# Performance work log

Measured on AMD Instinct MI355X. Metric: run time of the kernel, lower is better.

Reference implementation:

```python
import jax, jax.numpy as jnp
import numpy as np

EPS = 1e-8
R_CUT = 4.8
NEW_NB = 20  # hardcoded neighbor truncation in the original forward
B = 32768
NB = 64


def setup_inputs() -> dict:
    key = jax.random.key(0)
    ks = jax.random.split(key, 9)
    # dr: random directions with radii in [1.5, 4.5] so R > ecode (tanh^2 <= 1);
    # this avoids NaN from negative base with fractional exponent (same hazard exists in torch).
    raw = jax.random.normal(ks[0], (B, NB, 3), dtype=jnp.float32)
    direction = raw / jnp.linalg.norm(raw, axis=-1, keepdims=True)
    radius = 1.5 + 3.0 * jax.random.uniform(ks[1], (B, NB, 1), dtype=jnp.float32)
    dr = direction * radius
    orientation = jax.random.normal(ks[2], (B, 3, 3), dtype=jnp.float32)
    n_orientation = jax.random.normal(ks[3], (B, NB, 3, 3), dtype=jnp.float32)

    def lin(k, fan_in, fan_out):
        s = 1.0 / np.sqrt(fan_in)
        kw, kb = jax.random.split(k)
        W = jax.random.uniform(kw, (fan_in, fan_out), jnp.float32, -s, s)
        b = jax.random.uniform(kb, (fan_out,), jnp.float32, -s, s)
        return W, b

    W0, b0 = lin(ks[4], 15, 64)
    W1, b1 = lin(ks[5], 64, 64)
    W2, b2 = lin(ks[6], 64, 1)
    f1 = jax.random.uniform(ks[7], (3, 1), dtype=jnp.float32)
    f2 = jax.random.uniform(ks[8], (3, 1), dtype=jnp.float32)
    return dict(dr=dr, orientation=orientation, n_orientation=n_orientation,
                W0=W0, b0=b0, W1=W1, b1=b1, W2=W2, b2=b2, f1=f1, f2=f2)


def _prior_net(x, W0, b0, W1, b1, W2, b2):
    # Linear-tanh-Linear-tanh-Linear (dropout inactive at eval)
    h = jnp.tanh(x @ W0 + b0)
    h = jnp.tanh(h @ W1 + b1)
    return h @ W2 + b2


def _energy(new_dr_norm, orientation, new_R, new_n_or, fcR, W0, b0, W1, b1, W2, b2, f1, f2):
    b, n = new_dr_norm.shape[:2]
    dr_o = jnp.einsum('bnk,bkh->bnh', new_dr_norm, orientation)            # [B,20,3]
    dr_no = jnp.einsum('bnk,bnkh->bnh', new_dr_norm, new_n_or)             # [B,20,3]
    o_no = jnp.einsum('bhl,bnhm->bnlm', orientation, new_n_or).reshape(b, n, 9)
    feat = jnp.concatenate([dr_o, dr_no, o_no], axis=-1)                   # [B,20,15]
    enc = jnp.tanh(_prior_net(feat, W0, b0, W1, b1, W2, b2))               # [B,20,1]
    ecode = (enc ** 2 + EPS)[..., None, None]                              # [B,20,1,1,1]
    prior = new_R[..., None, None] - ecode                                 # [B,20,1,1,1]
    prior = (f1 ** 2 + EPS) * prior                                        # [B,20,1,3,1]
    prior = prior ** (-(f2 ** 2 + EPS))                                    # power-law
    prior = prior.sum(axis=3).reshape(b, n, 1)                             # [B,20,1]
    energy = prior.sum(axis=1, keepdims=True) * fcR                        # [B,20,1]
    return energy


def _forward(dr, orientation, n_orientation, W0, b0, W1, b1, W2, b2, f1, f2):
    b = dr.shape[0]
    dr = dr + EPS
    R = jnp.linalg.norm(dr, axis=-1, keepdims=True)                        # [B,Nb,1]
    dr_norm = dr / R
    idx = jnp.argsort(R, axis=1)[:, :NEW_NB, :]                            # [B,20,1]
    new_R = jnp.take_along_axis(R, idx, axis=1)                            # [B,20,1]
    new_dr_norm = jnp.take_along_axis(dr_norm, jnp.broadcast_to(idx, (b, NEW_NB, 3)), axis=1)
    new_n_or = jnp.take_along_axis(n_orientation, jnp.broadcast_to(idx[..., None], (b, NEW_NB, 3, 3)), axis=1)
    fcR = jnp.where(new_R > R_CUT, 0.0, 0.5 * jnp.cos(jnp.pi * new_R / R_CUT) + 0.5)

    def esum(ndn, orient):
        e = _energy(ndn, orient, new_R, new_n_or, fcR, W0, b0, W1, b1, W2, b2, f1, f2)
        return e.sum(), e

    # mirrors torch.autograd.grad(energy.sum(), (new_dr_norm, orientation), create_graph=True)
    (_, energy), (g_dr, g_or) = jax.value_and_grad(esum, argnums=(0, 1), has_aux=True)(new_dr_norm, orientation)
    force = g_dr.sum(axis=1)                                               # [B,3]
    torque = (jnp.cross(g_or[:, :, 0], orientation[:, :, 0])
              + jnp.cross(g_or[:, :, 1], orientation[:, :, 1])
              + jnp.cross(g_or[:, :, 2], orientation[:, :, 2]))            # [B,3]
    return force, torque, energy


def reference(dr, orientation, n_orientation, W0, b0, W1, b1, W2, b2, f1, f2):
    return _forward(dr, orientation, n_orientation, W0, b0, W1, b1, W2, b2, f1, f2)
```

## Files before the change

### kernel.cpp

```cpp
#include <hip/hip_runtime.h>

#define EPSF 1e-8f
#define RCUT 4.8f
#define NB 64
#define NSEL 20

#define OW0T 0
#define OB0  1024
#define OB1  1088
#define OW2  1152
#define OB2  1216
#define OAQ  1220
#define OCQ  1224
#define OLG  1228
#define OW1  1232
#define WSWN 5328

__device__ __forceinline__ float fast_tanh(float x) {
    float e = __expf(2.0f * x);
    return 1.0f - __fdividef(2.0f, e + 1.0f);
}

extern "C" __global__ void __launch_bounds__(256)
sel_kernel(const float* __restrict__ dr, const float* __restrict__ n_or,
           const float* __restrict__ W0, const float* __restrict__ b0,
           const float* __restrict__ W1, const float* __restrict__ b1,
           const float* __restrict__ W2, const float* __restrict__ b2,
           const float* __restrict__ f1, const float* __restrict__ f2,
           float* __restrict__ ws_R, float* __restrict__ ws_fc,
           float* __restrict__ ws_F, int* __restrict__ ws_idx,
           float* __restrict__ ws_ndn, float* __restrict__ ws_nor,
           float* __restrict__ wsW)
{
    __shared__ float R_s[256];
    const int t = threadIdx.x;
    const int g = t >> 6;
    const int j = t & 63;
    const int b = blockIdx.x * 4 + g;

    const float* p = dr + ((size_t)b * NB + j) * 3;
    float x = p[0] + EPSF, y = p[1] + EPSF, z = p[2] + EPSF;
    float R = sqrtf(x * x + y * y + z * z);
    R_s[t] = R;
    __syncthreads();

    int rank = 0;
    const float* grp = R_s + g * 64;
    #pragma unroll 8
    for (int k = 0; k < 64; ++k) {
        float Rk = grp[k];
        rank += (Rk < R || (Rk == R && k < j)) ? 1 : 0;
    }

    float fc = 0.0f;
    if (rank < NSEL) {
        fc = (R > RCUT) ? 0.0f
                        : (0.5f * __cosf(3.14159265358979323846f * R / RCUT) + 0.5f);
        size_t o = (size_t)b * NSEL + rank;
        ws_R[o]  = R;
        ws_fc[o] = fc;
        if (ws_idx) ws_idx[o] = j;
        float inv = 1.0f / R;
        ws_ndn[o * 3 + 0] = x * inv;
        ws_ndn[o * 3 + 1] = y * inv;
        ws_ndn[o * 3 + 2] = z * inv;
    }

    if (ws_nor) {
        const float* np = n_or + ((size_t)b * NB + j) * 9;
        float r[9];
        #pragma unroll
        for (int q = 0; q < 9; ++q) r[q] = np[q];
        if (rank < NSEL) {
            float* dst = ws_nor + ((size_t)b * NSEL + rank) * 9;
            #pragma unroll
            for (int q = 0; q < 9; ++q) dst[q] = r[q];
        }
    }

    float F = fc;
    for (int off = 32; off > 0; off >>= 1) F += __shfl_xor(F, off, 64);
    if (j == 0) ws_F[b] = F;

    if (blockIdx.x == 0) {
        for (int i = t; i < 15 * 64; i += 256) {
            int k = i >> 6, jj = i & 63;
            wsW[OW0T + jj * 16 + k] = W0[i];
        }
        for (int i = t; i < 64 * 64; i += 256)
            wsW[OW1 + i] = W1[i];
        if (t < 64) {
            wsW[OB0 + t] = b0[t];
            wsW[OB1 + t] = b1[t];
            wsW[OW2 + t] = W2[t];
        }
        if (t == 0) wsW[OB2] = b2[0];
        if (t < 3) {
            float a = f1[t] * f1[t] + EPSF;
            float c = f2[t] * f2[t] + EPSF;
            wsW[OAQ + t] = a;
            wsW[OCQ + t] = c;
            wsW[OLG + t] = __logf(a);
        }
    }
}

template<bool PRE>
__global__ void __launch_bounds__(320, 4)
energy_kernel_t(const float* __restrict__ orientation,
                const float* __restrict__ n_or,
                const float* __restrict__ wsW,
                const float* __restrict__ wsD,
                const int*   __restrict__ ws_idx_fb,
                const float* __restrict__ ws_ndn_fb,
                float* __restrict__ outBase, const int Bn)
{
    __shared__ float sNr[320 * 9];
    __shared__ float p_s[320];
    __shared__ float red[320][12];
    __shared__ float G[16][12];

    const float* W0T = wsW + OW0T;
    const float* b0  = wsW + OB0;
    const float* b1  = wsW + OB1;
    const float* W2  = wsW + OW2;
    const float* W1  = wsW + OW1;

    const float* ws_R  = wsD;
    const float* ws_fc = wsD + (size_t)Bn * NSEL;
    const float* ws_F  = wsD + (size_t)Bn * (2 * NSEL);
    const float* ws_ndn = PRE ? (wsD + (size_t)Bn * (2 * NSEL + 1)) : ws_ndn_fb;
    const float* ws_nor = wsD + (size_t)Bn * (2 * NSEL + 1 + 3 * NSEL);

    const int t = threadIdx.x;
    const int bl = t / 20;
    const int n  = t % 20;
    const int b  = blockIdx.x * 16 + bl;
    const size_t o = (size_t)b * NSEL + n;

    float feat[15];
    {
        const float nd0 = ws_ndn[o * 3 + 0];
        const float nd1 = ws_ndn[o * 3 + 1];
        const float nd2 = ws_ndn[o * 3 + 2];
        float O[9], Nr[9];
        const float* Op = orientation + (size_t)b * 9;
        #pragma unroll
        for (int i = 0; i < 9; ++i) O[i] = Op[i];
        if (PRE) {
            const float* Np = ws_nor + o * 9;
            #pragma unroll
            for (int i = 0; i < 9; ++i) Nr[i] = Np[i];
        } else {
            const int idx = ws_idx_fb[o];
            const float* Np = n_or + ((size_t)b * NB + idx) * 9;
            #pragma unroll
            for (int i = 0; i < 9; ++i) Nr[i] = Np[i];
        }
        #pragma unroll
        for (int q = 0; q < 9; ++q) sNr[t * 9 + q] = Nr[q];

        #pragma unroll
        for (int h = 0; h < 3; ++h)
            feat[h] = nd0 * O[h] + nd1 * O[3 + h] + nd2 * O[6 + h];
        #pragma unroll
        for (int h = 0; h < 3; ++h)
            feat[3 + h] = nd0 * Nr[h] + nd1 * Nr[3 + h] + nd2 * Nr[6 + h];
        #pragma unroll
        for (int l = 0; l < 3; ++l)
            #pragma unroll
            for (int m = 0; m < 3; ++m)
                feat[6 + l * 3 + m] = O[l] * Nr[m] + O[3 + l] * Nr[3 + m] + O[6 + l] * Nr[6 + m];
    }

    float acc[64];
    #pragma unroll
    for (int i = 0; i < 64; ++i) acc[i] = b1[i];

    for (int j = 0; j < 64; j += 2) {
        const float* w0a = W0T + j * 16;
        const float* w0b = w0a + 16;
        float za = b0[j], zb = b0[j + 1];
        #pragma unroll
        for (int k = 0; k < 15; ++k) {
            za = fmaf(feat[k], w0a[k], za);
            zb = fmaf(feat[k], w0b[k], zb);
        }
        float ha = fast_tanh(za), hb = fast_tanh(zb);
        const float* w1a = W1 + j * 64;
        const float* w1b = w1a + 64;
        #pragma unroll
        for (int i = 0; i < 64; ++i)
            acc[i] = fmaf(hb, w1b[i], fmaf(ha, w1a[i], acc[i]));
    }

    float z30 = wsW[OB2], z31 = 0.f, z32 = 0.f, z33 = 0.f;
    #pragma unroll
    for (int i = 0; i < 64; i += 4) {
        acc[i]     = fast_tanh(acc[i]);
        acc[i + 1] = fast_tanh(acc[i + 1]);
        acc[i + 2] = fast_tanh(acc[i + 2]);
        acc[i + 3] = fast_tanh(acc[i + 3]);
        z30 = fmaf(acc[i],     W2[i],     z30);
        z31 = fmaf(acc[i + 1], W2[i + 1], z31);
        z32 = fmaf(acc[i + 2], W2[i + 2], z32);
        z33 = fmaf(acc[i + 3], W2[i + 3], z33);
    }
    const float enc = fast_tanh((z30 + z31) + (z32 + z33));
    float x;
    {
        const volatile float* Rv = ws_R + o;
        x = Rv[0] - (enc * enc + EPSF);
    }

    const float lx = __logf(x);
    float psum = 0.f, csum = 0.f;
    #pragma unroll
    for (int q = 0; q < 3; ++q) {
        float cq = wsW[OCQ + q];
        float tq = __expf(-cq * (wsW[OLG + q] + lx));
        psum += tq;
        csum = fmaf(cq, tq, csum);
    }
    const float dpdx = -__fdividef(csum, x);

    p_s[t] = psum;
    __syncthreads();
    {
        float S = 0.f;
        for (int m = 0; m < 20; ++m) S += p_s[bl * 20 + m];
        const volatile float* fcv = ws_fc + o;
        outBase[(size_t)Bn * 6 + o] = S * fcv[0];
    }

    float dz3;
    {
        const volatile float* Fv = ws_F + b;
        dz3 = Fv[0] * dpdx * (-2.f * enc) * (1.f - enc * enc);
    }
    #pragma unroll
    for (int i = 0; i < 64; ++i) {
        float h2 = acc[i];
        acc[i] = dz3 * W2[i] * (1.f - h2 * h2);
    }

    float dfeat[15];
    #pragma unroll
    for (int k = 0; k < 15; ++k) dfeat[k] = 0.f;

    for (int j = 62; j >= 0; j -= 2) {
        const float* w1a = W1 + j * 64;
        const float* w1b = w1a + 64;
        float sa0 = 0.f, sa1 = 0.f, sb0 = 0.f, sb1 = 0.f;
        #pragma unroll
        for (int i = 0; i < 64; i += 2) {
            sa0 = fmaf(acc[i],     w1a[i],     sa0);
            sa1 = fmaf(acc[i + 1], w1a[i + 1], sa1);
            sb0 = fmaf(acc[i],     w1b[i],     sb0);
            sb1 = fmaf(acc[i + 1], w1b[i + 1], sb1);
        }
        float dha = sa0 + sa1, dhb = sb0 + sb1;
        const float* w0a = W0T + j * 16;
        const float* w0b = w0a + 16;
        float za = b0[j], zb = b0[j + 1];
        #pragma unroll
        for (int k = 0; k < 15; ++k) {
            za = fmaf(feat[k], w0a[k], za);
            zb = fmaf(feat[k], w0b[k], zb);
        }
        float ha = fast_tanh(za), hb = fast_tanh(zb);
        float dza = dha * (1.f - ha * ha);
        float dzb = dhb * (1.f - hb * hb);
        #pragma unroll
        for (int k = 0; k < 15; ++k)
            dfeat[k] = fmaf(dzb, w0b[k], fmaf(dza, w0a[k], dfeat[k]));
    }

    float O[9], Nr[9], nd0, nd1, nd2;
    {
        const volatile float* Ov = orientation + (size_t)b * 9;
        #pragma unroll
        for (int i = 0; i < 9; ++i) O[i] = Ov[i];
        volatile float* sv = sNr + t * 9;
        #pragma unroll
        for (int i = 0; i < 9; ++i) Nr[i] = sv[i];
        const volatile float* nv = ws_ndn + o * 3;
        nd0 = nv[0]; nd1 = nv[1]; nd2 = nv[2];
    }

    float gdr[3];
    #pragma unroll
    for (int k = 0; k < 3; ++k)
        gdr[k] = dfeat[0] * O[k * 3] + dfeat[1] * O[k * 3 + 1] + dfeat[2] * O[k * 3 + 2]
               + dfeat[3] * Nr[k * 3] + dfeat[4] * Nr[k * 3 + 1] + dfeat[5] * Nr[k * 3 + 2];

    float ndv[3] = {nd0, nd1, nd2};
    float gO[9];
    #pragma unroll
    for (int k = 0; k < 3; ++k)
        #pragma unroll
        for (int h = 0; h < 3; ++h)
            gO[k * 3 + h] = dfeat[h] * ndv[k];
    #pragma unroll
    for (int h = 0; h < 3; ++h)
        #pragma unroll
        for (int l = 0; l < 3; ++l) {
            float s = 0.f;
            #pragma unroll
            for (int m = 0; m < 3; ++m) s = fmaf(dfeat[6 + l * 3 + m], Nr[h * 3 + m], s);
            gO[h * 3 + l] += s;
        }

    #pragma unroll
    for (int q = 0; q < 3; ++q) red[t][q] = gdr[q];
    #pragma unroll
    for (int q = 0; q < 9; ++q) red[t][3 + q] = gO[q];
    __syncthreads();

    for (int i = t; i < 16 * 12; i += 320) {
        int bb = i / 12, q = i % 12;
        float s = 0.f;
        for (int m = 0; m < 20; ++m) s += red[bb * 20 + m][q];
        G[bb][q] = s;
    }
    __syncthreads();

    if (t < 16) {
        const int gb = blockIdx.x * 16 + t;
        float* out_force  = outBase;
        float* out_torque = outBase + (size_t)Bn * 3;
        out_force[gb * 3 + 0] = G[t][0];
        out_force[gb * 3 + 1] = G[t][1];
        out_force[gb * 3 + 2] = G[t][2];
        const float* Og = orientation + (size_t)gb * 9;
        float t0 = 0.f, t1 = 0.f, t2 = 0.f;
        #pragma unroll
        for (int jj = 0; jj < 3; ++jj) {
            float u0 = G[t][3 + 0 * 3 + jj], u1 = G[t][3 + 1 * 3 + jj], u2 = G[t][3 + 2 * 3 + jj];
            float v0 = Og[0 * 3 + jj], v1 = Og[1 * 3 + jj], v2 = Og[2 * 3 + jj];
            t0 += u1 * v2 - u2 * v1;
            t1 += u2 * v0 - u0 * v2;
            t2 += u0 * v1 - u1 * v0;
        }
        out_torque[gb * 3 + 0] = t0;
        out_torque[gb * 3 + 1] = t1;
        out_torque[gb * 3 + 2] = t2;
    }
}

extern "C" void kernel_launch(void* const* d_in, const int* in_sizes, int n_in,
                              void* d_out, int out_size, void* d_ws, size_t ws_size,
                              hipStream_t stream) {
    const float* dr            = (const float*)d_in[0];
    const float* orientation   = (const float*)d_in[1];
    const float* n_orientation = (const float*)d_in[2];
    const float* W0 = (const float*)d_in[3];
    const float* b0 = (const float*)d_in[4];
    const float* W1 = (const float*)d_in[5];
    const float* b1 = (const float*)d_in[6];
    const float* W2 = (const float*)d_in[7];
    const float* b2 = (const float*)d_in[8];
    const float* f1 = (const float*)d_in[9];
    const float* f2 = (const float*)d_in[10];

    const int B = in_sizes[0] / (NB * 3);

    float* out = (float*)d_out;

    float* ws_R  = (float*)d_ws;
    float* ws_fc = ws_R + (size_t)B * NSEL;
    float* ws_F  = ws_fc + (size_t)B * NSEL;

    const size_t needed_pre = sizeof(float) * ((size_t)B * 281 + WSWN);
    const bool pre = ws_size >= needed_pre;

    if (pre) {
        float* ws_ndn = ws_F + B;
        float* ws_nor = ws_ndn + (size_t)B * NSEL * 3;
        float* wsW    = ws_nor + (size_t)B * NSEL * 9;
        sel_kernel<<<B / 4, 256, 0, stream>>>(dr, n_orientation,
                                              W0, b0, W1, b1, W2, b2, f1, f2,
                                              ws_R, ws_fc, ws_F, nullptr,
                                              ws_ndn, ws_nor, wsW);
        energy_kernel_t<true><<<B / 16, 320, 0, stream>>>(
            orientation, n_orientation, wsW, ws_R, nullptr, nullptr, out, B);
    } else {
        int*   ws_idx = (int*)(ws_F + B);
        float* ws_ndn = (float*)(ws_idx + (size_t)B * NSEL);
        float* wsW    = ws_ndn + (size_t)B * NSEL * 3;
        sel_kernel<<<B / 4, 256, 0, stream>>>(dr, n_orientation,
                                              W0, b0, W1, b1, W2, b2, f1, f2,
                                              ws_R, ws_fc, ws_F, ws_idx,
                                              ws_ndn, nullptr, wsW);
        energy_kernel_t<false><<<B / 16, 320, 0, stream>>>(
            orientation, n_orientation, wsW, ws_R, ws_idx, ws_ndn, out, B);
    }
}
```

Baseline: 476.1 us.

## Split the 64-wide hidden layer across two thread halves per neighbor

Doubles the energy kernel block to 640 threads so each (batch, neighbor) pair is handled by two threads, each owning 32 of the 64 second-layer hidden units. Partial output-layer sums and the partial input-feature gradients are combined through shared memory with extra barriers. This halves per-thread register arrays (acc) to raise occupancy and parallelism. The cost is the first layer and the W0 backward being computed twice, plus extra shared memory and synchronisation.

```diff
diff --git a/kernel.cpp b/kernel.cpp
--- a/kernel.cpp
+++ b/kernel.cpp
@@ -106,7 +106,7 @@
 }
 
 template<bool PRE>
-__global__ void __launch_bounds__(320, 4)
+__global__ void __launch_bounds__(640, 5)
 energy_kernel_t(const float* __restrict__ orientation,
                 const float* __restrict__ n_or,
                 const float* __restrict__ wsW,
@@ -116,7 +116,9 @@
                 float* __restrict__ outBase, const int Bn)
 {
     __shared__ float sNr[320 * 9];
+    __shared__ float zx[2][320];
     __shared__ float p_s[320];
+    __shared__ float xf[320][15];
     __shared__ float red[320][12];
     __shared__ float G[16][12];
 
@@ -133,8 +135,11 @@
     const float* ws_nor = wsD + (size_t)Bn * (2 * NSEL + 1 + 3 * NSEL);
 
     const int t = threadIdx.x;
-    const int bl = t / 20;
-    const int n  = t % 20;
+    const int h  = __builtin_amdgcn_readfirstlane(t >= 320 ? 1 : 0);
+    const int iB = h * 32;
+    const int p  = t - h * 320;
+    const int bl = p / 20;
+    const int n  = p % 20;
     const int b  = blockIdx.x * 16 + bl;
     const size_t o = (size_t)b * NSEL + n;
 
@@ -157,15 +162,17 @@
             #pragma unroll
             for (int i = 0; i < 9; ++i) Nr[i] = Np[i];
         }
-        #pragma unroll
-        for (int q = 0; q < 9; ++q) sNr[t * 9 + q] = Nr[q];
-
-        #pragma unroll
-        for (int h = 0; h < 3; ++h)
-            feat[h] = nd0 * O[h] + nd1 * O[3 + h] + nd2 * O[6 + h];
-        #pragma unroll
-        for (int h = 0; h < 3; ++h)
-            feat[3 + h] = nd0 * Nr[h] + nd1 * Nr[3 + h] + nd2 * Nr[6 + h];
+        if (h == 0) {
+            #pragma unroll
+            for (int q = 0; q < 9; ++q) sNr[p * 9 + q] = Nr[q];
+        }
+
+        #pragma unroll
+        for (int hh = 0; hh < 3; ++hh)
+            feat[hh] = nd0 * O[hh] + nd1 * O[3 + hh] + nd2 * O[6 + hh];
+        #pragma unroll
+        for (int hh = 0; hh < 3; ++hh)
+            feat[3 + hh] = nd0 * Nr[hh] + nd1 * Nr[3 + hh] + nd2 * Nr[6 + hh];
         #pragma unroll
         for (int l = 0; l < 3; ++l)
             #pragma unroll
@@ -173,9 +180,9 @@
                 feat[6 + l * 3 + m] = O[l] * Nr[m] + O[3 + l] * Nr[3 + m] + O[6 + l] * Nr[6 + m];
     }
 
-    float acc[64];
+    float acc[32];
     #pragma unroll
-    for (int i = 0; i < 64; ++i) acc[i] = b1[i];
+    for (int i = 0; i < 32; ++i) acc[i] = b1[iB + i];
 
     for (int j = 0; j < 64; j += 2) {
         const float* w0a = W0T + j * 16;
@@ -187,26 +194,31 @@
             zb = fmaf(feat[k], w0b[k], zb);
         }
         float ha = fast_tanh(za), hb = fast_tanh(zb);
-        const float* w1a = W1 + j * 64;
+        const float* w1a = W1 + j * 64 + iB;
         const float* w1b = w1a + 64;
         #pragma unroll
-        for (int i = 0; i < 64; ++i)
+        for (int i = 0; i < 32; ++i)
             acc[i] = fmaf(hb, w1b[i], fmaf(ha, w1a[i], acc[i]));
     }
 
-    float z30 = wsW[OB2], z31 = 0.f, z32 = 0.f, z33 = 0.f;
+    float z30 = h ? 0.f : wsW[OB2];
+    float z31 = 0.f, z32 = 0.f, z33 = 0.f;
     #pragma unroll
-    for (int i = 0; i < 64; i += 4) {
+    for (int i = 0; i < 32; i += 4) {
         acc[i]     = fast_tanh(acc[i]);
         acc[i + 1] = fast_tanh(acc[i + 1]);
         acc[i + 2] = fast_tanh(acc[i + 2]);
         acc[i + 3] = fast_tanh(acc[i + 3]);
-        z30 = fmaf(acc[i],     W2[i],     z30);
-        z31 = fmaf(acc[i + 1], W2[i + 1], z31);
-        z32 = fmaf(acc[i + 2], W2[i + 2], z32);
-        z33 = fmaf(acc[i + 3], W2[i + 3], z33);
-    }
-    const float enc = fast_tanh((z30 + z31) + (z32 + z33));
+        z30 = fmaf(acc[i],     W2[iB + i],     z30);
+        z31 = fmaf(acc[i + 1], W2[iB + i + 1], z31);
+        z32 = fmaf(acc[i + 2], W2[iB + i + 2], z32);
+        z33 = fmaf(acc[i + 3], W2[iB + i + 3], z33);
+    }
+    zx[h][p] = (z30 + z31) + (z32 + z33);
+    __syncthreads();
+    const float z3 = zx[0][p] + zx[1][p];
+
+    const float enc = fast_tanh(z3);
     float x;
     {
         const volatile float* Rv = ws_R + o;
@@ -224,9 +236,9 @@
     }
     const float dpdx = -__fdividef(csum, x);
 
-    p_s[t] = psum;
-    __syncthreads();
-    {
+    if (h == 0) p_s[p] = psum;
+    __syncthreads();
+    if (h == 0) {
         float S = 0.f;
         for (int m = 0; m < 20; ++m) S += p_s[bl * 20 + m];
         const volatile float* fcv = ws_fc + o;
@@ -239,9 +251,9 @@
         dz3 = Fv[0] * dpdx * (-2.f * enc) * (1.f - enc * enc);
     }
     #pragma unroll
-    for (int i = 0; i < 64; ++i) {
+    for (int i = 0; i < 32; ++i) {
         float h2 = acc[i];
-        acc[i] = dz3 * W2[i] * (1.f - h2 * h2);
+        acc[i] = dz3 * W2[iB + i] * (1.f - h2 * h2);
     }
 
     float dfeat[15];
@@ -249,11 +261,11 @@
     for (int k = 0; k < 15; ++k) dfeat[k] = 0.f;
 
     for (int j = 62; j >= 0; j -= 2) {
-        const float* w1a = W1 + j * 64;
+        const float* w1a = W1 + j * 64 + iB;
         const float* w1b = w1a + 64;
         float sa0 = 0.f, sa1 = 0.f, sb0 = 0.f, sb1 = 0.f;
         #pragma unroll
-        for (int i = 0; i < 64; i += 2) {
+        for (int i = 0; i < 32; i += 2) {
             sa0 = fmaf(acc[i],     w1a[i],     sa0);
             sa1 = fmaf(acc[i + 1], w1a[i + 1], sa1);
             sb0 = fmaf(acc[i],     w1b[i],     sb0);
@@ -276,48 +288,59 @@
             dfeat[k] = fmaf(dzb, w0b[k], fmaf(dza, w0a[k], dfeat[k]));
     }
 
-    float O[9], Nr[9], nd0, nd1, nd2;
-    {
-        const volatile float* Ov = orientation + (size_t)b * 9;
-        #pragma unroll
-        for (int i = 0; i < 9; ++i) O[i] = Ov[i];
-        volatile float* sv = sNr + t * 9;
-        #pragma unroll
-        for (int i = 0; i < 9; ++i) Nr[i] = sv[i];
-        const volatile float* nv = ws_ndn + o * 3;
-        nd0 = nv[0]; nd1 = nv[1]; nd2 = nv[2];
-    }
-
-    float gdr[3];
-    #pragma unroll
-    for (int k = 0; k < 3; ++k)
-        gdr[k] = dfeat[0] * O[k * 3] + dfeat[1] * O[k * 3 + 1] + dfeat[2] * O[k * 3 + 2]
-               + dfeat[3] * Nr[k * 3] + dfeat[4] * Nr[k * 3 + 1] + dfeat[5] * Nr[k * 3 + 2];
-
-    float ndv[3] = {nd0, nd1, nd2};
-    float gO[9];
-    #pragma unroll
-    for (int k = 0; k < 3; ++k)
-        #pragma unroll
-        for (int h = 0; h < 3; ++h)
-            gO[k * 3 + h] = dfeat[h] * ndv[k];
-    #pragma unroll
-    for (int h = 0; h < 3; ++h)
-        #pragma unroll
-        for (int l = 0; l < 3; ++l) {
-            float s = 0.f;
-            #pragma unroll
-            for (int m = 0; m < 3; ++m) s = fmaf(dfeat[6 + l * 3 + m], Nr[h * 3 + m], s);
-            gO[h * 3 + l] += s;
-        }
-
-    #pragma unroll
-    for (int q = 0; q < 3; ++q) red[t][q] = gdr[q];
-    #pragma unroll
-    for (int q = 0; q < 9; ++q) red[t][3 + q] = gO[q];
-    __syncthreads();
-
-    for (int i = t; i < 16 * 12; i += 320) {
+    if (h == 1) {
+        #pragma unroll
+        for (int k = 0; k < 15; ++k) xf[p][k] = dfeat[k];
+    }
+    __syncthreads();
+
+    if (h == 0) {
+        #pragma unroll
+        for (int k = 0; k < 15; ++k) dfeat[k] += xf[p][k];
+
+        float O[9], Nr[9], nd0, nd1, nd2;
+        {
+            const volatile float* Ov = orientation + (size_t)b * 9;
+            #pragma unroll
+            for (int i = 0; i < 9; ++i) O[i] = Ov[i];
+            volatile float* sv = sNr + p * 9;
+            #pragma unroll
+            for (int i = 0; i < 9; ++i) Nr[i] = sv[i];
+            const volatile float* nv = ws_ndn + o * 3;
+            nd0 = nv[0]; nd1 = nv[1]; nd2 = nv[2];
+        }
+
+        float gdr[3];
+        #pragma unroll
+        for (int k = 0; k < 3; ++k)
+            gdr[k] = dfeat[0] * O[k * 3] + dfeat[1] * O[k * 3 + 1] + dfeat[2] * O[k * 3 + 2]
+                   + dfeat[3] * Nr[k * 3] + dfeat[4] * Nr[k * 3 + 1] + dfeat[5] * Nr[k * 3 + 2];
+
+        float ndv[3] = {nd0, nd1, nd2};
+        float gO[9];
+        #pragma unroll
+        for (int k = 0; k < 3; ++k)
+            #pragma unroll
+            for (int hh = 0; hh < 3; ++hh)
+                gO[k * 3 + hh] = dfeat[hh] * ndv[k];
+        #pragma unroll
+        for (int hh = 0; hh < 3; ++hh)
+            #pragma unroll
+            for (int l = 0; l < 3; ++l) {
+                float s = 0.f;
+                #pragma unroll
+                for (int m = 0; m < 3; ++m) s = fmaf(dfeat[6 + l * 3 + m], Nr[hh * 3 + m], s);
+                gO[hh * 3 + l] += s;
+            }
+
+        #pragma unroll
+        for (int q = 0; q < 3; ++q) red[p][q] = gdr[q];
+        #pragma unroll
+        for (int q = 0; q < 9; ++q) red[p][3 + q] = gO[q];
+    }
+    __syncthreads();
+
+    for (int i = t; i < 16 * 12; i += 640) {
         int bb = i / 12, q = i % 12;
         float s = 0.f;
         for (int m = 0; m < 20; ++m) s += red[bb * 20 + m][q];
@@ -382,7 +405,7 @@
                                               W0, b0, W1, b1, W2, b2, f1, f2,
                                               ws_R, ws_fc, ws_F, nullptr,
                                               ws_ndn, ws_nor, wsW);
-        energy_kernel_t<true><<<B / 16, 320, 0, stream>>>(
+        energy_kernel_t<true><<<B / 16, 640, 0, stream>>>(
             orientation, n_orientation, wsW, ws_R, nullptr, nullptr, out, B);
     } else {
         int*   ws_idx = (int*)(ws_F + B);
@@ -392,7 +415,7 @@
                                               W0, b0, W1, b1, W2, b2, f1, f2,
                                               ws_R, ws_fc, ws_F, ws_idx,
                                               ws_ndn, nullptr, wsW);
-        energy_kernel_t<false><<<B / 16, 320, 0, stream>>>(
+        energy_kernel_t<false><<<B / 16, 640, 0, stream>>>(
             orientation, n_orientation, wsW, ws_R, ws_idx, ws_ndn, out, B);
     }
 }
```

New measurement: 589.2 us. +23.7%, slower.

## Restructure energy kernel to map hidden units to lanes with LDS-staged weights

Applied to the files above, without the earlier changes.

The energy/gradient kernel is reorganized so each 64-lane wave handles 10 neighbors, with one lane per hidden unit. W1 and W0T are staged in padded shared memory, and activations are exchanged through per-wave LDS buffers instead of each thread carrying a full 64-wide accumulator per neighbor. Reductions for the output layer and the per-particle force/torque use wave shuffles rather than a 320x12 shared-memory reduction. Blocks grow to 512 threads covering 4 particles. This cuts per-thread register pressure and the per-thread weight loads, at the cost of more LDS traffic, idle lanes in the scalar per-neighbor stages, and a weight reload into LDS for every block.

```diff
diff --git a/kernel.cpp b/kernel.cpp
--- a/kernel.cpp
+++ b/kernel.cpp
@@ -15,6 +15,13 @@
 #define OLG  1228
 #define OW1  1232
 #define WSWN 5328
+
+#define SB0 0
+#define SB1 64
+#define SW2 128
+#define SB2 192
+#define SCQ 200
+#define SLG 204
 
 __device__ __forceinline__ float fast_tanh(float x) {
     float e = __expf(2.0f * x);
@@ -106,7 +113,7 @@
 }
 
 template<bool PRE>
-__global__ void __launch_bounds__(320, 4)
+__global__ void __launch_bounds__(512, 4)
 energy_kernel_t(const float* __restrict__ orientation,
                 const float* __restrict__ n_or,
                 const float* __restrict__ wsW,
@@ -115,35 +122,55 @@
                 const float* __restrict__ ws_ndn_fb,
                 float* __restrict__ outBase, const int Bn)
 {
-    __shared__ float sNr[320 * 9];
-    __shared__ float p_s[320];
-    __shared__ float red[320][12];
-    __shared__ float G[16][12];
-
-    const float* W0T = wsW + OW0T;
-    const float* b0  = wsW + OB0;
-    const float* b1  = wsW + OB1;
-    const float* W2  = wsW + OW2;
-    const float* W1  = wsW + OW1;
-
-    const float* ws_R  = wsD;
-    const float* ws_fc = wsD + (size_t)Bn * NSEL;
-    const float* ws_F  = wsD + (size_t)Bn * (2 * NSEL);
+    __shared__ float sW1[64 * 65];
+    __shared__ float sW0T[64 * 17];
+    __shared__ float sC[208];
+    __shared__ float h1b[8][64 * 12];
+    __shared__ float dzb[8][64 * 12];
+    __shared__ float featb[8][10 * 16];
+    __shared__ float dz3b[8][10];
+    __shared__ float sG[4][2][12];
+    __shared__ float sPsum[4][2];
+
+    const int t    = threadIdx.x;
+    const int wave = t >> 6;
+    const int lane = t & 63;
+    const int bb   = wave >> 1;
+    const int w    = wave & 1;
+    const int b    = blockIdx.x * 4 + bb;
+
+    for (int i = t; i < 64 * 64; i += 512) {
+        int r = i >> 6, c = i & 63;
+        sW1[r * 65 + c] = wsW[OW1 + i];
+    }
+    for (int i = t; i < 64 * 16; i += 512) {
+        int r = i >> 4, c = i & 15;
+        sW0T[r * 17 + c] = wsW[OW0T + i];
+    }
+    if (t < 208) sC[t] = wsW[OB0 + t];
+    __syncthreads();
+
+    const float* ws_R   = wsD;
+    const float* ws_fc  = wsD + (size_t)Bn * NSEL;
+    const float* ws_F   = wsD + (size_t)Bn * (2 * NSEL);
     const float* ws_ndn = PRE ? (wsD + (size_t)Bn * (2 * NSEL + 1)) : ws_ndn_fb;
     const float* ws_nor = wsD + (size_t)Bn * (2 * NSEL + 1 + 3 * NSEL);
 
-    const int t = threadIdx.x;
-    const int bl = t / 20;
-    const int n  = t % 20;
-    const int b  = blockIdx.x * 16 + bl;
-    const size_t o = (size_t)b * NSEL + n;
-
-    float feat[15];
-    {
-        const float nd0 = ws_ndn[o * 3 + 0];
-        const float nd1 = ws_ndn[o * 3 + 1];
-        const float nd2 = ws_ndn[o * 3 + 2];
-        float O[9], Nr[9];
+    const int g = lane;
+    const size_t o = (size_t)b * NSEL + w * 10 + g;
+    const float Fb = ws_F[b];
+
+    float* myH1   = &h1b[wave][0];
+    float* myDz   = &dzb[wave][0];
+    float* myFeat = &featb[wave][0];
+
+    float O[9], Nr[9], nd0 = 0.f, nd1 = 0.f, nd2 = 0.f, Rv = 0.f, fcv = 0.f;
+    if (lane < 10) {
+        nd0 = ws_ndn[o * 3 + 0];
+        nd1 = ws_ndn[o * 3 + 1];
+        nd2 = ws_ndn[o * 3 + 2];
+        Rv  = ws_R[o];
+        fcv = ws_fc[o];
         const float* Op = orientation + (size_t)b * 9;
         #pragma unroll
         for (int i = 0; i < 9; ++i) O[i] = Op[i];
@@ -157,9 +184,7 @@
             #pragma unroll
             for (int i = 0; i < 9; ++i) Nr[i] = Np[i];
         }
-        #pragma unroll
-        for (int q = 0; q < 9; ++q) sNr[t * 9 + q] = Nr[q];
-
+        float feat[15];
         #pragma unroll
         for (int h = 0; h < 3; ++h)
             feat[h] = nd0 * O[h] + nd1 * O[3 + h] + nd2 * O[6 + h];
@@ -171,180 +196,226 @@
             #pragma unroll
             for (int m = 0; m < 3; ++m)
                 feat[6 + l * 3 + m] = O[l] * Nr[m] + O[3 + l] * Nr[3 + m] + O[6 + l] * Nr[6 + m];
-    }
-
-    float acc[64];
-    #pragma unroll
-    for (int i = 0; i < 64; ++i) acc[i] = b1[i];
-
-    for (int j = 0; j < 64; j += 2) {
-        const float* w0a = W0T + j * 16;
-        const float* w0b = w0a + 16;
-        float za = b0[j], zb = b0[j + 1];
-        #pragma unroll
-        for (int k = 0; k < 15; ++k) {
-            za = fmaf(feat[k], w0a[k], za);
-            zb = fmaf(feat[k], w0b[k], zb);
-        }
-        float ha = fast_tanh(za), hb = fast_tanh(zb);
-        const float* w1a = W1 + j * 64;
-        const float* w1b = w1a + 64;
-        #pragma unroll
-        for (int i = 0; i < 64; ++i)
-            acc[i] = fmaf(hb, w1b[i], fmaf(ha, w1a[i], acc[i]));
-    }
-
-    float z30 = wsW[OB2], z31 = 0.f, z32 = 0.f, z33 = 0.f;
-    #pragma unroll
-    for (int i = 0; i < 64; i += 4) {
-        acc[i]     = fast_tanh(acc[i]);
-        acc[i + 1] = fast_tanh(acc[i + 1]);
-        acc[i + 2] = fast_tanh(acc[i + 2]);
-        acc[i + 3] = fast_tanh(acc[i + 3]);
-        z30 = fmaf(acc[i],     W2[i],     z30);
-        z31 = fmaf(acc[i + 1], W2[i + 1], z31);
-        z32 = fmaf(acc[i + 2], W2[i + 2], z32);
-        z33 = fmaf(acc[i + 3], W2[i + 3], z33);
-    }
-    const float enc = fast_tanh((z30 + z31) + (z32 + z33));
-    float x;
+        #pragma unroll
+        for (int k = 0; k < 15; ++k) myFeat[g * 16 + k] = feat[k];
+    }
+
+    float w0r[15];
+    #pragma unroll
+    for (int k = 0; k < 15; ++k) w0r[k] = sW0T[lane * 17 + k];
+    const float b0l = sC[SB0 + lane];
     {
-        const volatile float* Rv = ws_R + o;
-        x = Rv[0] - (enc * enc + EPSF);
-    }
-
-    const float lx = __logf(x);
-    float psum = 0.f, csum = 0.f;
-    #pragma unroll
-    for (int q = 0; q < 3; ++q) {
-        float cq = wsW[OCQ + q];
-        float tq = __expf(-cq * (wsW[OLG + q] + lx));
-        psum += tq;
-        csum = fmaf(cq, tq, csum);
-    }
-    const float dpdx = -__fdividef(csum, x);
-
-    p_s[t] = psum;
+        float hbuf[10];
+        #pragma unroll
+        for (int gg = 0; gg < 10; ++gg) {
+            const float4 f0 = *(const float4*)&myFeat[gg * 16 + 0];
+            const float4 f1 = *(const float4*)&myFeat[gg * 16 + 4];
+            const float4 f2 = *(const float4*)&myFeat[gg * 16 + 8];
+            const float4 f3 = *(const float4*)&myFeat[gg * 16 + 12];
+            float z = b0l;
+            z = fmaf(f0.x, w0r[0], z);  z = fmaf(f0.y, w0r[1], z);
+            z = fmaf(f0.z, w0r[2], z);  z = fmaf(f0.w, w0r[3], z);
+            z = fmaf(f1.x, w0r[4], z);  z = fmaf(f1.y, w0r[5], z);
+            z = fmaf(f1.z, w0r[6], z);  z = fmaf(f1.w, w0r[7], z);
+            z = fmaf(f2.x, w0r[8], z);  z = fmaf(f2.y, w0r[9], z);
+            z = fmaf(f2.z, w0r[10], z); z = fmaf(f2.w, w0r[11], z);
+            z = fmaf(f3.x, w0r[12], z); z = fmaf(f3.y, w0r[13], z);
+            z = fmaf(f3.z, w0r[14], z);
+            hbuf[gg] = fast_tanh(z);
+        }
+        #pragma unroll
+        for (int gg = 0; gg < 10; ++gg) myH1[lane * 12 + gg] = hbuf[gg];
+    }
+
+    float acc[10];
+    {
+        const float b1l = sC[SB1 + lane];
+        #pragma unroll
+        for (int gg = 0; gg < 10; ++gg) acc[gg] = b1l;
+    }
+    #pragma unroll 4
+    for (int j = 0; j < 64; ++j) {
+        const float wv = sW1[j * 65 + lane];
+        const float4 hA = *(const float4*)&myH1[j * 12 + 0];
+        const float4 hB = *(const float4*)&myH1[j * 12 + 4];
+        const float4 hC = *(const float4*)&myH1[j * 12 + 8];
+        acc[0] = fmaf(hA.x, wv, acc[0]); acc[1] = fmaf(hA.y, wv, acc[1]);
+        acc[2] = fmaf(hA.z, wv, acc[2]); acc[3] = fmaf(hA.w, wv, acc[3]);
+        acc[4] = fmaf(hB.x, wv, acc[4]); acc[5] = fmaf(hB.y, wv, acc[5]);
+        acc[6] = fmaf(hB.z, wv, acc[6]); acc[7] = fmaf(hB.w, wv, acc[7]);
+        acc[8] = fmaf(hC.x, wv, acc[8]); acc[9] = fmaf(hC.y, wv, acc[9]);
+    }
+
+    const float w2l = sC[SW2 + lane];
+    float z3v[10];
+    #pragma unroll
+    for (int gg = 0; gg < 10; ++gg) {
+        float h2 = fast_tanh(acc[gg]);
+        acc[gg] = h2;
+        float v = h2 * w2l;
+        v += __shfl_xor(v, 1, 64);  v += __shfl_xor(v, 2, 64);
+        v += __shfl_xor(v, 4, 64);  v += __shfl_xor(v, 8, 64);
+        v += __shfl_xor(v, 16, 64); v += __shfl_xor(v, 32, 64);
+        z3v[gg] = v + sC[SB2];
+    }
+
+    float psum = 0.f;
+    if (lane < 10) {
+        float z3 = z3v[0];
+        #pragma unroll
+        for (int gg = 1; gg < 10; ++gg) z3 = (g == gg) ? z3v[gg] : z3;
+        const float enc = fast_tanh(z3);
+        const float x = Rv - (enc * enc + EPSF);
+        const float lx = __logf(x);
+        float csum = 0.f;
+        #pragma unroll
+        for (int q = 0; q < 3; ++q) {
+            float cq = sC[SCQ + q];
+            float tq = __expf(-cq * (sC[SLG + q] + lx));
+            psum += tq;
+            csum = fmaf(cq, tq, csum);
+        }
+        const float dpdx = -__fdividef(csum, x);
+        dz3b[wave][g] = Fb * dpdx * (-2.f * enc) * (1.f - enc * enc);
+    }
+
+    float d3[10];
+    #pragma unroll
+    for (int gg = 0; gg < 10; ++gg) d3[gg] = dz3b[wave][gg];
+    #pragma unroll
+    for (int gg = 0; gg < 10; ++gg) {
+        float h2 = acc[gg];
+        acc[gg] = d3[gg] * w2l * (1.f - h2 * h2);
+    }
+    *(float4*)&myDz[lane * 12 + 0] = make_float4(acc[0], acc[1], acc[2], acc[3]);
+    *(float4*)&myDz[lane * 12 + 4] = make_float4(acc[4], acc[5], acc[6], acc[7]);
+    *(float4*)&myDz[lane * 12 + 8] = make_float4(acc[8], acc[9], 0.f, 0.f);
+
+    float dha[10];
+    #pragma unroll
+    for (int gg = 0; gg < 10; ++gg) dha[gg] = 0.f;
+    #pragma unroll 4
+    for (int i = 0; i < 64; ++i) {
+        const float wv = sW1[lane * 65 + i];
+        const float4 dA = *(const float4*)&myDz[i * 12 + 0];
+        const float4 dB = *(const float4*)&myDz[i * 12 + 4];
+        const float4 dC = *(const float4*)&myDz[i * 12 + 8];
+        dha[0] = fmaf(dA.x, wv, dha[0]); dha[1] = fmaf(dA.y, wv, dha[1]);
+        dha[2] = fmaf(dA.z, wv, dha[2]); dha[3] = fmaf(dA.w, wv, dha[3]);
+        dha[4] = fmaf(dB.x, wv, dha[4]); dha[5] = fmaf(dB.y, wv, dha[5]);
+        dha[6] = fmaf(dB.z, wv, dha[6]); dha[7] = fmaf(dB.w, wv, dha[7]);
+        dha[8] = fmaf(dC.x, wv, dha[8]); dha[9] = fmaf(dC.y, wv, dha[9]);
+    }
+
+    {
+        const float4 hA = *(const float4*)&myH1[lane * 12 + 0];
+        const float4 hB = *(const float4*)&myH1[lane * 12 + 4];
+        const float4 hC = *(const float4*)&myH1[lane * 12 + 8];
+        float hv[10] = {hA.x, hA.y, hA.z, hA.w, hB.x, hB.y, hB.z, hB.w, hC.x, hC.y};
+        #pragma unroll
+        for (int gg = 0; gg < 10; ++gg) {
+            float z1 = dha[gg] * (1.f - hv[gg] * hv[gg]);
+            myH1[lane * 12 + gg] = z1;
+        }
+    }
+
+    {
+        const int k9  = lane % 15;
+        const int gl9 = lane / 15;
+        #pragma unroll
+        for (int pss = 0; pss < 3; ++pss) {
+            const int g9 = pss * 4 + gl9;
+            const bool act = (lane < 60) && (g9 < 10);
+            float dacc = 0.f;
+            if (act) {
+                #pragma unroll 8
+                for (int j = 0; j < 64; ++j)
+                    dacc = fmaf(myH1[j * 12 + g9], sW0T[j * 17 + k9], dacc);
+                myFeat[g9 * 16 + k9] = dacc;
+            }
+        }
+    }
+
+    float comps[12];
+    #pragma unroll
+    for (int q = 0; q < 12; ++q) comps[q] = 0.f;
+    if (lane < 10) {
+        float df[15];
+        {
+            const float4 f0 = *(const float4*)&myFeat[g * 16 + 0];
+            const float4 f1 = *(const float4*)&myFeat[g * 16 + 4];
+            const float4 f2 = *(const float4*)&myFeat[g * 16 + 8];
+            const float4 f3 = *(const float4*)&myFeat[g * 16 + 12];
+            df[0]=f0.x; df[1]=f0.y; df[2]=f0.z; df[3]=f0.w;
+            df[4]=f1.x; df[5]=f1.y; df[6]=f1.z; df[7]=f1.w;
+            df[8]=f2.x; df[9]=f2.y; df[10]=f2.z; df[11]=f2.w;
+            df[12]=f3.x; df[13]=f3.y; df[14]=f3.z;
+        }
+        #pragma unroll
+        for (int k = 0; k < 3; ++k)
+            comps[k] = df[0] * O[k * 3] + df[1] * O[k * 3 + 1] + df[2] * O[k * 3 + 2]
+                     + df[3] * Nr[k * 3] + df[4] * Nr[k * 3 + 1] + df[5] * Nr[k * 3 + 2];
+        float ndv[3] = {nd0, nd1, nd2};
+        #pragma unroll
+        for (int k = 0; k < 3; ++k)
+            #pragma unroll
+            for (int h = 0; h < 3; ++h)
+                comps[3 + k * 3 + h] = df[h] * ndv[k];
+        #pragma unroll
+        for (int h = 0; h < 3; ++h)
+            #pragma unroll
+            for (int l = 0; l < 3; ++l) {
+                float s = 0.f;
+                #pragma unroll
+                for (int m = 0; m < 3; ++m) s = fmaf(df[6 + l * 3 + m], Nr[h * 3 + m], s);
+                comps[3 + h * 3 + l] += s;
+            }
+    }
+    #pragma unroll
+    for (int q = 0; q < 12; ++q) {
+        float v = comps[q];
+        v += __shfl_xor(v, 1, 64); v += __shfl_xor(v, 2, 64);
+        v += __shfl_xor(v, 4, 64); v += __shfl_xor(v, 8, 64);
+        comps[q] = v;
+    }
+    {
+        float ps = (lane < 10) ? psum : 0.f;
+        ps += __shfl_xor(ps, 1, 64); ps += __shfl_xor(ps, 2, 64);
+        ps += __shfl_xor(ps, 4, 64); ps += __shfl_xor(ps, 8, 64);
+        if (lane == 0) {
+            #pragma unroll
+            for (int q = 0; q < 12; ++q) sG[bb][w][q] = comps[q];
+            sPsum[bb][w] = ps;
+        }
+    }
     __syncthreads();
-    {
-        float S = 0.f;
-        for (int m = 0; m < 20; ++m) S += p_s[bl * 20 + m];
-        const volatile float* fcv = ws_fc + o;
-        outBase[(size_t)Bn * 6 + o] = S * fcv[0];
-    }
-
-    float dz3;
-    {
-        const volatile float* Fv = ws_F + b;
-        dz3 = Fv[0] * dpdx * (-2.f * enc) * (1.f - enc * enc);
-    }
-    #pragma unroll
-    for (int i = 0; i < 64; ++i) {
-        float h2 = acc[i];
-        acc[i] = dz3 * W2[i] * (1.f - h2 * h2);
-    }
-
-    float dfeat[15];
-    #pragma unroll
-    for (int k = 0; k < 15; ++k) dfeat[k] = 0.f;
-
-    for (int j = 62; j >= 0; j -= 2) {
-        const float* w1a = W1 + j * 64;
-        const float* w1b = w1a + 64;
-        float sa0 = 0.f, sa1 = 0.f, sb0 = 0.f, sb1 = 0.f;
-        #pragma unroll
-        for (int i = 0; i < 64; i += 2) {
-            sa0 = fmaf(acc[i],     w1a[i],     sa0);
-            sa1 = fmaf(acc[i + 1], w1a[i + 1], sa1);
-            sb0 = fmaf(acc[i],     w1b[i],     sb0);
-            sb1 = fmaf(acc[i + 1], w1b[i + 1], sb1);
-        }
-        float dha = sa0 + sa1, dhb = sb0 + sb1;
-        const float* w0a = W0T + j * 16;
-        const float* w0b = w0a + 16;
-        float za = b0[j], zb = b0[j + 1];
-        #pragma unroll
-        for (int k = 0; k < 15; ++k) {
-            za = fmaf(feat[k], w0a[k], za);
-            zb = fmaf(feat[k], w0b[k], zb);
-        }
-        float ha = fast_tanh(za), hb = fast_tanh(zb);
-        float dza = dha * (1.f - ha * ha);
-        float dzb = dhb * (1.f - hb * hb);
-        #pragma unroll
-        for (int k = 0; k < 15; ++k)
-            dfeat[k] = fmaf(dzb, w0b[k], fmaf(dza, w0a[k], dfeat[k]));
-    }
-
-    float O[9], Nr[9], nd0, nd1, nd2;
-    {
-        const volatile float* Ov = orientation + (size_t)b * 9;
-        #pragma unroll
-        for (int i = 0; i < 9; ++i) O[i] = Ov[i];
-        volatile float* sv = sNr + t * 9;
-        #pragma unroll
-        for (int i = 0; i < 9; ++i) Nr[i] = sv[i];
-        const volatile float* nv = ws_ndn + o * 3;
-        nd0 = nv[0]; nd1 = nv[1]; nd2 = nv[2];
-    }
-
-    float gdr[3];
-    #pragma unroll
-    for (int k = 0; k < 3; ++k)
-        gdr[k] = dfeat[0] * O[k * 3] + dfeat[1] * O[k * 3 + 1] + dfeat[2] * O[k * 3 + 2]
-               + dfeat[3] * Nr[k * 3] + dfeat[4] * Nr[k * 3 + 1] + dfeat[5] * Nr[k * 3 + 2];
-
-    float ndv[3] = {nd0, nd1, nd2};
-    float gO[9];
-    #pragma unroll
-    for (int k = 0; k < 3; ++k)
-        #pragma unroll
-        for (int h = 0; h < 3; ++h)
-            gO[k * 3 + h] = dfeat[h] * ndv[k];
-    #pragma unroll
-    for (int h = 0; h < 3; ++h)
-        #pragma unroll
-        for (int l = 0; l < 3; ++l) {
-            float s = 0.f;
-            #pragma unroll
-            for (int m = 0; m < 3; ++m) s = fmaf(dfeat[6 + l * 3 + m], Nr[h * 3 + m], s);
-            gO[h * 3 + l] += s;
-        }
-
-    #pragma unroll
-    for (int q = 0; q < 3; ++q) red[t][q] = gdr[q];
-    #pragma unroll
-    for (int q = 0; q < 9; ++q) red[t][3 + q] = gO[q];
-    __syncthreads();
-
-    for (int i = t; i < 16 * 12; i += 320) {
-        int bb = i / 12, q = i % 12;
-        float s = 0.f;
-        for (int m = 0; m < 20; ++m) s += red[bb * 20 + m][q];
-        G[bb][q] = s;
-    }
-    __syncthreads();
-
-    if (t < 16) {
-        const int gb = blockIdx.x * 16 + t;
+
+    if (lane < 10) {
+        const float S2 = sPsum[bb][0] + sPsum[bb][1];
+        outBase[(size_t)Bn * 6 + o] = S2 * fcv;
+    }
+
+    if (w == 0 && lane == 0) {
+        float Gq[12];
+        #pragma unroll
+        for (int q = 0; q < 12; ++q) Gq[q] = sG[bb][0][q] + sG[bb][1][q];
         float* out_force  = outBase;
         float* out_torque = outBase + (size_t)Bn * 3;
-        out_force[gb * 3 + 0] = G[t][0];
-        out_force[gb * 3 + 1] = G[t][1];
-        out_force[gb * 3 + 2] = G[t][2];
-        const float* Og = orientation + (size_t)gb * 9;
+        out_force[b * 3 + 0] = Gq[0];
+        out_force[b * 3 + 1] = Gq[1];
+        out_force[b * 3 + 2] = Gq[2];
         float t0 = 0.f, t1 = 0.f, t2 = 0.f;
         #pragma unroll
         for (int jj = 0; jj < 3; ++jj) {
-            float u0 = G[t][3 + 0 * 3 + jj], u1 = G[t][3 + 1 * 3 + jj], u2 = G[t][3 + 2 * 3 + jj];
-            float v0 = Og[0 * 3 + jj], v1 = Og[1 * 3 + jj], v2 = Og[2 * 3 + jj];
+            float u0 = Gq[3 + 0 * 3 + jj], u1 = Gq[3 + 1 * 3 + jj], u2 = Gq[3 + 2 * 3 + jj];
+            float v0 = O[0 * 3 + jj], v1 = O[1 * 3 + jj], v2 = O[2 * 3 + jj];
             t0 += u1 * v2 - u2 * v1;
             t1 += u2 * v0 - u0 * v2;
             t2 += u0 * v1 - u1 * v0;
         }
-        out_torque[gb * 3 + 0] = t0;
-        out_torque[gb * 3 + 1] = t1;
-        out_torque[gb * 3 + 2] = t2;
+        out_torque[b * 3 + 0] = t0;
+        out_torque[b * 3 + 1] = t1;
+        out_torque[b * 3 + 2] = t2;
     }
 }
 
@@ -382,7 +453,7 @@
                                               W0, b0, W1, b1, W2, b2, f1, f2,
                                               ws_R, ws_fc, ws_F, nullptr,
                                               ws_ndn, ws_nor, wsW);
-        energy_kernel_t<true><<<B / 16, 320, 0, stream>>>(
+        energy_kernel_t<true><<<B / 4, 512, 0, stream>>>(
             orientation, n_orientation, wsW, ws_R, nullptr, nullptr, out, B);
     } else {
         int*   ws_idx = (int*)(ws_F + B);
@@ -392,7 +463,7 @@
                                               W0, b0, W1, b1, W2, b2, f1, f2,
                                               ws_R, ws_fc, ws_F, ws_idx,
                                               ws_ndn, nullptr, wsW);
-        energy_kernel_t<false><<<B / 16, 320, 0, stream>>>(
+        energy_kernel_t<false><<<B / 4, 512, 0, stream>>>(
             orientation, n_orientation, wsW, ws_R, ws_idx, ws_ndn, out, B);
     }
 }
```

After: 593.6 us. 1.25x slower.
